# Optimization experiments

Hardware: AMD Instinct MI355X
Metric: run time of the kernel (lower is better)

The kernel has to match this reference:

```python
import jax, jax.numpy as jnp
import numpy as np
import math

M_MICRO = 8    # n_micro
CELLS = 1024   # cells per micro engine (n_cells // n_micro)
DIM = 512      # hidden_dim (complex state dim)
IN_DIM = 512   # input_dim == hidden_dim so torch's F.interpolate branch is skipped


def _build_neighbors(n):
    """Hypercube bit-flip + ring topology, deduped, padded to max degree."""
    n_bits = max(1, int(math.ceil(math.log2(n))))
    lists = []
    for i in range(n):
        s = set()
        for b in range(n_bits):
            j = i ^ (1 << b)
            if 0 <= j < n:
                s.add(j)
        s.add((i + 1) % n)
        s.add((i - 1) % n)
        lists.append(sorted(s))
    K = max(len(l) for l in lists)
    idx = np.zeros((n, K), dtype=np.int32)
    mask = np.zeros((n, K), dtype=np.float32)
    for i, l in enumerate(lists):
        idx[i, : len(l)] = l
        mask[i, : len(l)] = 1.0
    return idx, mask


def _forward(x, step, amp0, phase0, phase_vel, nbr_idx, nbr_mask, macro_h0,
             w_ih, b_ih, w_hh, b_hh, wq, bq, wk, bk, wv, bv, out_w, out_b):
    sig = x.reshape(-1)                    # [DIM]; input_dim == dim -> no interpolation
    t = step * 0.1
    states0 = amp0 * jnp.exp(1j * phase0)  # complex64 [M, n, d]

    def micro_step(st, pv):
        # phase-velocity rotation
        st = st * jnp.exp(1j * (pv * 0.1))
        ang = jnp.angle(st)
        nb_s = st[nbr_idx]                 # [n, K, d] neighbor gather
        nb_a = ang[nbr_idx]
        coupling = jnp.cos(ang[:, None, :] - nb_a)
        interf = jnp.sum(coupling * nb_s * nbr_mask[:, :, None], axis=1) * 0.1
        cnt = jnp.maximum(nbr_mask.sum(axis=1), 1.0)
        new = 0.7 * st + 0.3 * interf / cnt[:, None]
        # category morphism from strongest neighbor (selected on pre-interference states)
        absum = jnp.abs(st).sum(axis=-1)
        score = jnp.where(nbr_mask > 0, absum[nbr_idx], -jnp.inf)
        sel = jnp.argmax(score, axis=1)
        midx = jnp.take_along_axis(nbr_idx, sel[:, None], axis=1)[:, 0]
        src = st[midx]
        morph = jnp.abs(src) * jnp.exp(1j * (jnp.angle(new) - jnp.angle(src)))
        new = new + 0.02 * morph
        # global wave modulation
        i_arr = jnp.arange(new.shape[0], dtype=jnp.float32)
        wave = 0.02 * jnp.sin(t + 2.0 * math.pi * i_arr / new.shape[0])
        new = new * (1.0 + wave)[:, None]
        # signal phase perturbation (per-cell decaying scale)
        sig_norm = sig / (jnp.abs(sig).max() + 1e-8)
        pp = sig_norm * (math.pi * 0.1)
        scale = 0.1 / (1.0 + 0.1 * i_arr)
        newang = jnp.angle(new) + pp[None, :] * scale[:, None]
        # amplitude renormalization
        amp = jnp.abs(new)
        amp = amp / (amp.max(axis=-1, keepdims=True) + 1e-8)
        return amp * jnp.exp(1j * newang)

    states = jax.vmap(micro_step)(states0, phase_vel)  # [M, n, d]
    # micro outputs and coherences are .detach()'ed / .item()'ed in torch
    micro_out = jax.lax.stop_gradient(jnp.abs(states).mean(axis=1))          # [M, d]
    coh = jax.lax.stop_gradient(
        jnp.abs(jnp.exp(1j * jnp.angle(states)).mean(axis=1)).mean(axis=1))  # [M]
    # GRUCell (torch gate order: r, z, n)
    gx = micro_out @ w_ih.T + b_ih
    gh = macro_h0 @ w_hh.T + b_hh
    rx, zx, nx = jnp.split(gx, 3, axis=1)
    rh, zh, nh = jnp.split(gh, 3, axis=1)
    r = jax.nn.sigmoid(rx + rh)
    z = jax.nn.sigmoid(zx + zh)
    ng = jnp.tanh(nx + r * nh)
    h = jax.lax.stop_gradient((1.0 - z) * ng + z * macro_h0)  # detached macro hiddens
    H = h.shape[1]
    Q = h @ wq.T + bq
    K = h @ wk.T + bk
    V = h @ wv.T + bv
    scores = (Q @ K.T) / math.sqrt(H)
    scores = scores * (0.5 + 0.5 * coh[None, :] * coh[:, None])
    attn = jax.nn.softmax(scores, axis=-1)
    attended = (attn @ V).mean(axis=0, keepdims=True)  # [1, H]
    # faction sync/debate (updates hidden state; feeds only tension here)
    n_f = 4
    fs = h.shape[0] // n_f
    hh = h.reshape(n_f, fs, -1)
    hh = 0.85 * hh + 0.15 * hh.mean(axis=1, keepdims=True)
    if step > 5:
        go = hh.mean(axis=1).mean(axis=0)
        dc = max(1, fs // 4)
        hh = hh.at[:, :dc].set(0.85 * hh[:, :dc] + 0.15 * go)
    h2 = hh.reshape(h.shape)
    pred = attended @ out_w.T + out_b  # [1, IN_DIM]
    tension = jnp.var(h2, ddof=1)      # torch .var() is unbiased
    return pred, tension


def setup_inputs():
    key = jax.random.key(0)
    k = jax.random.split(key, 20)
    M, n, d, H, IN = M_MICRO, CELLS, DIM, DIM, IN_DIM
    amp0 = jax.random.uniform(k[0], (M, n, d)) * 0.5 + 0.5
    base = jnp.linspace(0.0, 2.0 * math.pi, d)
    gidx = jnp.arange(M * n, dtype=jnp.float32).reshape(M, n)
    off = 2.0 * math.pi * gidx / (n * 8)
    phase0 = base[None, None, :] + off[..., None] + jax.random.normal(k[1], (M, n, d)) * 0.3
    phase_vel = jax.random.normal(k[2], (M, n, d)) * 0.05
    nbr_idx, nbr_mask = _build_neighbors(n)
    macro_h0 = jax.random.normal(k[3], (M, H)) * 0.1
    s = 1.0 / math.sqrt(H)
    u = lambda kk, shape: jax.random.uniform(kk, shape, minval=-s, maxval=s)
    return {
        "x": jax.random.normal(k[4], (1, IN)),
        "step": 0,
        "amp0": amp0, "phase0": phase0, "phase_vel": phase_vel,
        "nbr_idx": jnp.asarray(nbr_idx), "nbr_mask": jnp.asarray(nbr_mask),
        "macro_h0": macro_h0,
        "w_ih": u(k[5], (3 * H, H)), "b_ih": u(k[6], (3 * H,)),
        "w_hh": u(k[7], (3 * H, H)), "b_hh": u(k[8], (3 * H,)),
        "wq": u(k[9], (H, H)), "bq": u(k[10], (H,)),
        "wk": u(k[11], (H, H)), "bk": u(k[12], (H,)),
        "wv": u(k[13], (H, H)), "bv": u(k[14], (H,)),
        "out_w": u(k[15], (IN, H)), "out_b": u(k[16], (IN,)),
    }


def reference(x, step, amp0, phase0, phase_vel, nbr_idx, nbr_mask, macro_h0,
              w_ih, b_ih, w_hh, b_hh, wq, bq, wk, bk, wv, bv, out_w, out_b):
    return _forward(x, step, amp0, phase0, phase_vel, nbr_idx, nbr_mask, macro_h0,
                    w_ih, b_ih, w_hh, b_hh, wq, bq, wk, bk, wv, bv, out_w, out_b)
```

## Files before the change

### kernel.cpp

```cpp
#include <hip/hip_runtime.h>
#include <math.h>

#define M_  8
#define N_  1024
#define D_  512
#define H_  512
#define PI_ 3.14159265358979323846f

static const size_t OFF_ABS = 0;
static const size_t OFF_SIG = OFF_ABS + 8192;
static const size_t OFF_PA  = OFF_SIG + 64;
static const size_t OFF_PZR = OFF_PA  + (size_t)M_*64*D_;
static const size_t OFF_PZI = OFF_PZR + (size_t)M_*64*D_;
static const size_t OFF_MO  = OFF_PZI + (size_t)M_*64*D_;
static const size_t OFF_COH = OFF_MO  + (size_t)M_*D_;
static const size_t OFF_H   = OFF_COH + 64;
static const size_t OFF_Q   = OFF_H   + (size_t)M_*H_;
static const size_t OFF_K   = OFF_Q   + (size_t)M_*H_;
static const size_t OFF_V   = OFF_K   + (size_t)M_*H_;
static const size_t OFF_ATT = OFF_V   + (size_t)M_*H_;

__device__ __forceinline__ void ld8(float* d, const float* __restrict__ p, int lane) {
    const float4* p4 = reinterpret_cast<const float4*>(p);
    float4 v0 = p4[2 * lane], v1 = p4[2 * lane + 1];
    d[0] = v0.x; d[1] = v0.y; d[2] = v0.z; d[3] = v0.w;
    d[4] = v1.x; d[5] = v1.y; d[6] = v1.z; d[7] = v1.w;
}


__global__ void prep_kernel(const float* __restrict__ amp0, const float* __restrict__ x,
                            float* __restrict__ absum, float* __restrict__ sigmax) {
    const int lane = threadIdx.x;
    if (blockIdx.x < M_ * N_) {
        float v[8];
        ld8(v, amp0 + (size_t)blockIdx.x * D_, lane);
        float acc = ((v[0] + v[1]) + (v[2] + v[3])) + ((v[4] + v[5]) + (v[6] + v[7]));
        for (int off = 32; off; off >>= 1) acc += __shfl_down(acc, off);
        if (lane == 0) absum[blockIdx.x] = acc;
    } else {
        float v[8];
        ld8(v, x, lane);
        float mx = 0.f;
        #pragma unroll
        for (int s = 0; s < 8; ++s) mx = fmaxf(mx, fabsf(v[s]));
        for (int off = 32; off; off >>= 1) mx = fmaxf(mx, __shfl_down(mx, off));
        if (lane == 0) *sigmax = mx;
    }
}

__global__ __launch_bounds__(512) void micro_kernel(
    const float* __restrict__ amp0, const float* __restrict__ phase0,
    const float* __restrict__ pv, const float* __restrict__ x,
    const float* __restrict__ sigmax_p, const int* __restrict__ nbr_idx,
    const float* __restrict__ nbr_mask, const int* __restrict__ step_p,
    const float* __restrict__ absum,
    float* __restrict__ pA, float* __restrict__ pZr, float* __restrict__ pZi, int K)
{
    const int m = blockIdx.x & 7;
    const int g = blockIdx.x >> 3;
    const int wid  = threadIdx.x >> 6;
    const int lane = threadIdx.x & 63;

    __shared__ float accA[D_], accZr[D_], accZi[D_];
    for (int idx = threadIdx.x; idx < D_; idx += 512) { accA[idx] = 0.f; accZr[idx] = 0.f; accZi[idx] = 0.f; }
    __syncthreads();

    const float t  = 0.1f * (float)(*step_p);
    const float sm = *sigmax_p;
    const int j0 = lane * 8;

    float pp[8];
    ld8(pp, x, lane);
    #pragma unroll
    for (int s = 0; s < 8; ++s) pp[s] = pp[s] / (sm + 1e-8f) * (PI_ * 0.1f);

    const size_t mrow = (size_t)m * N_;
    float sA[8], sZr[8], sZi[8];
    #pragma unroll
    for (int s = 0; s < 8; ++s) { sA[s] = 0.f; sZr[s] = 0.f; sZi[s] = 0.f; }

    for (int cc = 0; cc < 2; ++cc) {
        const int i = (g << 4) + (wid << 1) + cc;

        float SA[8], SB[8], SC[8];
        #pragma unroll
        for (int s = 0; s < 8; ++s) { SA[s] = 0.f; SB[s] = 0.f; SC[s] = 0.f; }
        float cnt = 0.f, best = -1e30f; int midx = 0;

        for (int k = 0; k < K; ++k) {
            const int   nb = nbr_idx[i * K + k];
            const float w  = nbr_mask[i * K + k];
            if (w > 0.f) {
                const size_t noff = (mrow + nb) * (size_t)D_;
                float an[8], phn[8], pvn[8];
                ld8(an, amp0 + noff, lane);
                ld8(phn, phase0 + noff, lane);
                ld8(pvn, pv + noff, lane);
                #pragma unroll
                for (int s = 0; s < 8; ++s) {
                    const float th = fmaf(0.1f, pvn[s], phn[s]);
                    const float cn = __cosf(th), sn = __sinf(th);
                    const float ac = an[s] * cn, as_ = an[s] * sn;
                    SA[s] = fmaf(ac, cn, SA[s]);
                    SB[s] = fmaf(ac, sn, SB[s]);
                    SC[s] = fmaf(as_, sn, SC[s]);
                }
                cnt += w;
                const float sc = absum[mrow + nb];
                if (sc > best) { best = sc; midx = nb; }
            }
        }
        const float f = 0.03f / fmaxf(cnt, 1.f);

        const size_t ooff = (mrow + i) * (size_t)D_;
        float a[8], ph[8], pw[8], nre[8], nim[8];
        ld8(a, amp0 + ooff, lane); ld8(ph, phase0 + ooff, lane); ld8(pw, pv + ooff, lane);
        #pragma unroll
        for (int s = 0; s < 8; ++s) {
            const float th = fmaf(0.1f, pw[s], ph[s]);
            const float c = __cosf(th), sn = __sinf(th);
            nre[s] = 0.7f * a[s] * c  + f * (c * SA[s] + sn * SB[s]);
            nim[s] = 0.7f * a[s] * sn + f * (c * SB[s] + sn * SC[s]);
        }

        const size_t soff = (mrow + midx) * (size_t)D_;
        ld8(a, amp0 + soff, lane); ld8(ph, phase0 + soff, lane); ld8(pw, pv + soff, lane);
        #pragma unroll
        for (int s = 0; s < 8; ++s) {
            const float th = fmaf(0.1f, pw[s], ph[s]);
            const float c = __cosf(th), sn = __sinf(th);
            const float sre = a[s] * c, sim = a[s] * sn;
            const float inv = __builtin_amdgcn_rcpf(sqrtf(nre[s]*nre[s] + nim[s]*nim[s]));
            const float mre = (nre[s] * sre + nim[s] * sim) * inv;
            const float mim = (nim[s] * sre - nre[s] * sim) * inv;
            nre[s] = fmaf(0.02f, mre, nre[s]);
            nim[s] = fmaf(0.02f, mim, nim[s]);
        }

        const float wf = 1.f + 0.02f * __sinf(t + 2.f * PI_ * (float)i / (float)N_);
        const float scale_i = 0.1f / (1.f + 0.1f * (float)i);

        float ampn[8], rm = 0.f;
        #pragma unroll
        for (int s = 0; s < 8; ++s) {
            nre[s] *= wf; nim[s] *= wf;
            ampn[s] = sqrtf(nre[s]*nre[s] + nim[s]*nim[s]);
            rm = fmaxf(rm, ampn[s]);
        }
        #pragma unroll
        for (int off = 1; off < 64; off <<= 1) rm = fmaxf(rm, __shfl_xor(rm, off));
        const float rinv = __builtin_amdgcn_rcpf(rm + 1e-8f);

        #pragma unroll
        for (int s = 0; s < 8; ++s) {
            const float anorm = ampn[s] * rinv;
            const float iamp  = __builtin_amdgcn_rcpf(ampn[s]);
            const float ure = nre[s] * iamp, uim = nim[s] * iamp;
            const float d  = pp[s] * scale_i;
            const float d2 = d * d;
            const float cd = 1.f - 0.5f * d2;
            const float sd = d * (1.f - 0.16666667f * d2);
            sA[s]  += anorm;
            sZr[s] += ure * cd - uim * sd;
            sZi[s] += ure * sd + uim * cd;
        }
    }

    #pragma unroll
    for (int s = 0; s < 8; ++s) {
        atomicAdd(&accA[j0 + s],  sA[s]);
        atomicAdd(&accZr[j0 + s], sZr[s]);
        atomicAdd(&accZi[j0 + s], sZi[s]);
    }
    __syncthreads();
    const int j = threadIdx.x;
    const size_t pidx = ((size_t)(m * 64 + g)) * D_ + j;
    pA[pidx]  = accA[j];
    pZr[pidx] = accZr[j];
    pZi[pidx] = accZi[j];
}

__global__ void reduce_kernel(const float* __restrict__ pA,
                              const float* __restrict__ pZr,
                              const float* __restrict__ pZi,
                              float* __restrict__ micro_out,
                              float* __restrict__ coh) {
    const int m = blockIdx.x, j = threadIdx.x;
    float sa = 0.f, zr = 0.f, zi = 0.f;
    for (int g = 0; g < 64; ++g) {
        const size_t idx = ((size_t)m * 64 + g) * D_ + j;
        sa += pA[idx]; zr += pZr[idx]; zi += pZi[idx];
    }
    micro_out[m * D_ + j] = sa * (1.f / (float)N_);
    const float mag = sqrtf(zr * zr + zi * zi) * (1.f / (float)N_);
    __shared__ float red[D_];
    red[j] = mag;
    __syncthreads();
    for (int s = D_/2; s > 0; s >>= 1) {
        if (j < s) red[j] += red[j + s];
        __syncthreads();
    }
    if (j == 0) coh[m] = red[0] / (float)D_;
}

__global__ __launch_bounds__(256) void macro_kernel(
    const float* __restrict__ mo, const float* __restrict__ h0,
    const float* __restrict__ w_ih, const float* __restrict__ b_ih,
    const float* __restrict__ w_hh, const float* __restrict__ b_hh,
    float* __restrict__ h)
{
    __shared__ float vx[M_ * H_], vh[M_ * H_];
    for (int idx = threadIdx.x; idx < M_ * H_; idx += 256) { vx[idx] = mo[idx]; vh[idx] = h0[idx]; }
    __syncthreads();
    const int wid = threadIdx.x >> 6, lane = threadIdx.x & 63;
    const int d = (blockIdx.x << 2) + wid;
    float wr[6][8];
    #pragma unroll
    for (int rr = 0; rr < 3; ++rr) {
        const size_t row = (size_t)(d + rr * H_) * H_;
        #pragma unroll
        for (int kk = 0; kk < 8; ++kk) {
            wr[rr][kk]     = w_ih[row + kk * 64 + lane];
            wr[rr + 3][kk] = w_hh[row + kk * 64 + lane];
        }
    }
    const float br = b_ih[d], bz = b_ih[d + H_], bn = b_ih[d + 2 * H_];
    const float dr = b_hh[d], dz = b_hh[d + H_], dn = b_hh[d + 2 * H_];
    for (int m = 0; m < M_; ++m) {
        float acc[6] = {0.f, 0.f, 0.f, 0.f, 0.f, 0.f};
        #pragma unroll
        for (int kk = 0; kk < 8; ++kk) {
            const float xm = vx[m * H_ + kk * 64 + lane];
            const float hm = vh[m * H_ + kk * 64 + lane];
            acc[0] = fmaf(wr[0][kk], xm, acc[0]);
            acc[1] = fmaf(wr[1][kk], xm, acc[1]);
            acc[2] = fmaf(wr[2][kk], xm, acc[2]);
            acc[3] = fmaf(wr[3][kk], hm, acc[3]);
            acc[4] = fmaf(wr[4][kk], hm, acc[4]);
            acc[5] = fmaf(wr[5][kk], hm, acc[5]);
        }
        #pragma unroll
        for (int off = 32; off; off >>= 1)
            #pragma unroll
            for (int q = 0; q < 6; ++q) acc[q] += __shfl_down(acc[q], off);
        if (lane == 0) {
            const float r  = 1.f / (1.f + expf(-(acc[0] + br + acc[3] + dr)));
            const float z  = 1.f / (1.f + expf(-(acc[1] + bz + acc[4] + dz)));
            const float ng = tanhf(acc[2] + bn + r * (acc[5] + dn));
            h[m * H_ + d] = (1.f - z) * ng + z * vh[m * H_ + d];
        }
    }
}

__global__ void qkv_kernel(const float* __restrict__ h,
                           const float* __restrict__ wq, const float* __restrict__ bq,
                           const float* __restrict__ wk, const float* __restrict__ bk,
                           const float* __restrict__ wv, const float* __restrict__ bv,
                           float* __restrict__ Q, float* __restrict__ Kk, float* __restrict__ V) {
    __shared__ float hv[M_ * H_];
    for (int idx = threadIdx.x; idx < M_ * H_; idx += blockDim.x) hv[idx] = h[idx];
    __syncthreads();
    const int gr = (blockIdx.x << 2) + (threadIdx.x >> 6);
    const int lane = threadIdx.x & 63;
    const int which = gr / H_, r = gr % H_;
    const float* W = (which == 0) ? wq : ((which == 1) ? wk : wv);
    const float* B = (which == 0) ? bq : ((which == 1) ? bk : bv);
    float* O       = (which == 0) ? Q  : ((which == 1) ? Kk : V);
    float wvv[8];
    #pragma unroll
    for (int kk = 0; kk < 8; ++kk) wvv[kk] = W[(size_t)r * H_ + kk * 64 + lane];
    for (int m = 0; m < M_; ++m) {
        float acc = 0.f;
        #pragma unroll
        for (int kk = 0; kk < 8; ++kk) acc = fmaf(wvv[kk], hv[m * H_ + kk * 64 + lane], acc);
        for (int off = 32; off; off >>= 1) acc += __shfl_down(acc, off);
        if (lane == 0) O[m * H_ + r] = acc + B[r];
    }
}

__global__ void attn_faction_kernel(const float* __restrict__ Q, const float* __restrict__ Kk,
                                    const float* __restrict__ V, const float* __restrict__ coh,
                                    const float* __restrict__ h, const int* __restrict__ step_p,
                                    float* __restrict__ attended, float* __restrict__ out_tension) {
    const int tid = threadIdx.x;
    {
        const int j = tid;
        const int step = *step_p;
        float h2[M_];
        #pragma unroll
        for (int ff = 0; ff < 4; ++ff) {
            const float a = h[(2*ff) * H_ + j], b = h[(2*ff+1) * H_ + j];
            const float mn = 0.5f * (a + b);
            h2[2*ff]   = 0.85f * a + 0.15f * mn;
            h2[2*ff+1] = 0.85f * b + 0.15f * mn;
        }
        if (step > 5) {
            float go = 0.f;
            #pragma unroll
            for (int m = 0; m < M_; ++m) go += h2[m];
            go *= (1.f / (float)M_);
            #pragma unroll
            for (int ff = 0; ff < 4; ++ff) h2[2*ff] = 0.85f * h2[2*ff] + 0.15f * go;
        }
        float sum = 0.f, sq = 0.f;
        #pragma unroll
        for (int m = 0; m < M_; ++m) { sum += h2[m]; sq = fmaf(h2[m], h2[m], sq); }
        __shared__ float rs[D_], rq[D_];
        rs[j] = sum; rq[j] = sq;
        __syncthreads();
        for (int s = D_/2; s > 0; s >>= 1) {
            if (j < s) { rs[j] += rs[j + s]; rq[j] += rq[j + s]; }
            __syncthreads();
        }
        if (j == 0) {
            const float Nt = (float)(M_ * H_);
            const float mean = rs[0] / Nt;
            out_tension[0] = (rq[0] - Nt * mean * mean) / (Nt - 1.f);
        }
        __syncthreads();
    }
    __shared__ float sc[M_][M_];
    __shared__ float colw[M_];
    const int a = tid >> 6, lane = tid & 63;
    for (int b = 0; b < M_; ++b) {
        float acc = 0.f;
        #pragma unroll
        for (int kk = 0; kk < 8; ++kk) acc = fmaf(Q[a * H_ + kk * 64 + lane], Kk[b * H_ + kk * 64 + lane], acc);
        for (int off = 32; off; off >>= 1) acc += __shfl_down(acc, off);
        if (lane == 0) sc[a][b] = acc * rsqrtf((float)H_) * (0.5f + 0.5f * coh[a] * coh[b]);
    }
    __syncthreads();
    if (tid < M_) {
        float mx = -1e30f;
        for (int b = 0; b < M_; ++b) mx = fmaxf(mx, sc[tid][b]);
        float e[M_], smm = 0.f;
        for (int b = 0; b < M_; ++b) { e[b] = expf(sc[tid][b] - mx); smm += e[b]; }
        for (int b = 0; b < M_; ++b) sc[tid][b] = e[b] / smm;
    }
    __syncthreads();
    if (tid < M_) {
        float sum = 0.f;
        for (int a2 = 0; a2 < M_; ++a2) sum += sc[a2][tid];
        colw[tid] = sum * (1.f / (float)M_);
    }
    __syncthreads();
    float acc = 0.f;
    #pragma unroll
    for (int b = 0; b < M_; ++b) acc = fmaf(colw[b], V[b * H_ + tid], acc);
    attended[tid] = acc;
}

__global__ void pred_kernel(const float* __restrict__ attended,
                            const float* __restrict__ out_w, const float* __restrict__ out_b,
                            float* __restrict__ pred) {
    __shared__ float av[H_];
    for (int idx = threadIdx.x; idx < H_; idx += blockDim.x) av[idx] = attended[idx];
    __syncthreads();
    const int p = (blockIdx.x << 2) + (threadIdx.x >> 6);
    const int lane = threadIdx.x & 63;
    float acc = 0.f;
    #pragma unroll
    for (int kk = 0; kk < 8; ++kk) acc = fmaf(av[kk * 64 + lane], out_w[(size_t)p * H_ + kk * 64 + lane], acc);
    for (int off = 32; off; off >>= 1) acc += __shfl_down(acc, off);
    if (lane == 0) pred[p] = acc + out_b[p];
}


extern "C" void kernel_launch(void* const* d_in, const int* in_sizes, int n_in,
                              void* d_out, int out_size, void* d_ws, size_t ws_size,
                              hipStream_t stream) {
    const float* x      = (const float*)d_in[0];
    const int*   step   = (const int*)  d_in[1];
    const float* amp0   = (const float*)d_in[2];
    const float* phase0 = (const float*)d_in[3];
    const float* pvel   = (const float*)d_in[4];
    const int*   nbr_i  = (const int*)  d_in[5];
    const float* nbr_m  = (const float*)d_in[6];
    const float* h0     = (const float*)d_in[7];
    const float* w_ih   = (const float*)d_in[8];
    const float* b_ih   = (const float*)d_in[9];
    const float* w_hh   = (const float*)d_in[10];
    const float* b_hh   = (const float*)d_in[11];
    const float* wq     = (const float*)d_in[12];
    const float* bq     = (const float*)d_in[13];
    const float* wk     = (const float*)d_in[14];
    const float* bk     = (const float*)d_in[15];
    const float* wv     = (const float*)d_in[16];
    const float* bv     = (const float*)d_in[17];
    const float* out_w  = (const float*)d_in[18];
    const float* out_b  = (const float*)d_in[19];
    float* out = (float*)d_out;

    const int K = in_sizes[5] / N_;

    float* ws   = (float*)d_ws;
    float* wABS = ws + OFF_ABS;
    float* wSIG = ws + OFF_SIG;
    float* wPA  = ws + OFF_PA;
    float* wPZR = ws + OFF_PZR;
    float* wPZI = ws + OFF_PZI;
    float* wMO  = ws + OFF_MO;
    float* wCOH = ws + OFF_COH;
    float* wH   = ws + OFF_H;
    float* wQ   = ws + OFF_Q;
    float* wK   = ws + OFF_K;
    float* wV   = ws + OFF_V;
    float* wATT = ws + OFF_ATT;

    prep_kernel<<<M_ * N_ + 1, 64, 0, stream>>>(amp0, x, wABS, wSIG);
    micro_kernel<<<512, 512, 0, stream>>>(amp0, phase0, pvel, x, wSIG, nbr_i, nbr_m, step,
                                          wABS, wPA, wPZR, wPZI, K);
    reduce_kernel<<<M_, D_, 0, stream>>>(wPA, wPZR, wPZI, wMO, wCOH);
    macro_kernel<<<128, 256, 0, stream>>>(wMO, h0, w_ih, b_ih, w_hh, b_hh, wH);
    qkv_kernel<<<384, 256, 0, stream>>>(wH, wq, bq, wk, bk, wv, bv, wQ, wK, wV);
    attn_faction_kernel<<<1, 512, 0, stream>>>(wQ, wK, wV, wCOH, wH, step, wATT, out + 512);
    pred_kernel<<<128, 256, 0, stream>>>(wATT, out_w, out_b, out);
}
```

Baseline: 227.0 us.

## Precompute half-precision cos/sin table and fuse partial reductions via atomics

A prep pass now computes the rotated phase's cos/sin once per element and stores it as packed half2, so the micro kernel reads amp plus one half2 stream instead of recomputing trig from phase and velocity for every neighbour visit. The per-row absolute sums are computed inline with a wavefront reduction, so the separate absum pass goes away. Partial sums are accumulated straight into global buffers with atomics, which drops the reduce kernel, and coherence is computed inside the attention kernel. A fallback path keeps the fp32 recompute when the workspace is too small. The cost is an extra full-size half2 table write and read, fp16 rounding of cos/sin, and global atomic contention.

```diff
diff --git a/kernel.cpp b/kernel.cpp
--- a/kernel.cpp
+++ b/kernel.cpp
@@ -1,4 +1,5 @@
 #include <hip/hip_runtime.h>
+#include <hip/hip_fp16.h>
 #include <math.h>
 
 #define M_  8
@@ -7,210 +8,358 @@
 #define H_  512
 #define PI_ 3.14159265358979323846f
 
-static const size_t OFF_ABS = 0;
-static const size_t OFF_SIG = OFF_ABS + 8192;
-static const size_t OFF_PA  = OFF_SIG + 64;
-static const size_t OFF_PZR = OFF_PA  + (size_t)M_*64*D_;
-static const size_t OFF_PZI = OFF_PZR + (size_t)M_*64*D_;
-static const size_t OFF_MO  = OFF_PZI + (size_t)M_*64*D_;
-static const size_t OFF_COH = OFF_MO  + (size_t)M_*D_;
-static const size_t OFF_H   = OFF_COH + 64;
+static const size_t OFF_CHS = 0;
+static const size_t OFF_SIG = OFF_CHS + (size_t)M_*N_*D_;
+static const size_t OFF_MA  = OFF_SIG + 64;
+static const size_t OFF_MZR = OFF_MA  + (size_t)M_*D_;
+static const size_t OFF_MZI = OFF_MZR + (size_t)M_*D_;
+static const size_t OFF_H   = OFF_MZI + (size_t)M_*D_;
 static const size_t OFF_Q   = OFF_H   + (size_t)M_*H_;
 static const size_t OFF_K   = OFF_Q   + (size_t)M_*H_;
 static const size_t OFF_V   = OFF_K   + (size_t)M_*H_;
 static const size_t OFF_ATT = OFF_V   + (size_t)M_*H_;
-
-__device__ __forceinline__ void ld8(float* d, const float* __restrict__ p, int lane) {
-    const float4* p4 = reinterpret_cast<const float4*>(p);
-    float4 v0 = p4[2 * lane], v1 = p4[2 * lane + 1];
-    d[0] = v0.x; d[1] = v0.y; d[2] = v0.z; d[3] = v0.w;
-    d[4] = v1.x; d[5] = v1.y; d[6] = v1.z; d[7] = v1.w;
-}
-
-
-__global__ void prep_kernel(const float* __restrict__ amp0, const float* __restrict__ x,
-                            float* __restrict__ absum, float* __restrict__ sigmax) {
-    const int lane = threadIdx.x;
-    if (blockIdx.x < M_ * N_) {
+static const size_t FAST_FLOATS = OFF_ATT + 512;
+static const size_t FB_SIG = 0;
+static const size_t FB_MA  = FB_SIG + 64;
+static const size_t FB_MZR = FB_MA  + (size_t)M_*D_;
+static const size_t FB_MZI = FB_MZR + (size_t)M_*D_;
+static const size_t FB_H   = FB_MZI + (size_t)M_*D_;
+static const size_t FB_Q   = FB_H   + (size_t)M_*H_;
+static const size_t FB_K   = FB_Q   + (size_t)M_*H_;
+static const size_t FB_V   = FB_K   + (size_t)M_*H_;
+static const size_t FB_ATT = FB_V   + (size_t)M_*H_;
+
+struct F8   { float4 a, b; };
+struct H2x8 { __half2 h[8]; };
+
+__device__ __forceinline__ void unp8(float* d, const F8& v) {
+    d[0]=v.a.x; d[1]=v.a.y; d[2]=v.a.z; d[3]=v.a.w;
+    d[4]=v.b.x; d[5]=v.b.y; d[6]=v.b.z; d[7]=v.b.w;
+}
+
+
+__global__ __launch_bounds__(256) void prep_kernel(const float* __restrict__ phase0,
+                                                   const float* __restrict__ pv,
+                                                   const float* __restrict__ x,
+                                                   __half2* __restrict__ chs,
+                                                   float* __restrict__ acczero,
+                                                   float* __restrict__ sigmax) {
+    const int bid = blockIdx.x, tid = threadIdx.x;
+    if (bid < 2048) {
+        const size_t e = ((size_t)bid * 256 + tid) * 8;
+        float ph[8], pw[8];
+        unp8(ph, *reinterpret_cast<const F8*>(phase0 + e));
+        unp8(pw, *reinterpret_cast<const F8*>(pv + e));
+        H2x8 out;
+        #pragma unroll
+        for (int s = 0; s < 8; ++s) {
+            const float th = fmaf(0.1f, pw[s], ph[s]);
+            out.h[s] = __floats2half2_rn(__cosf(th), __sinf(th));
+        }
+        *reinterpret_cast<H2x8*>(chs + e) = out;
+        if (bid < 6) {
+            F8 z; z.a = make_float4(0.f,0.f,0.f,0.f); z.b = z.a;
+            *reinterpret_cast<F8*>(acczero + (size_t)bid * 2048 + (size_t)tid * 8) = z;
+        }
+    } else if (tid < 64) {
         float v[8];
-        ld8(v, amp0 + (size_t)blockIdx.x * D_, lane);
-        float acc = ((v[0] + v[1]) + (v[2] + v[3])) + ((v[4] + v[5]) + (v[6] + v[7]));
-        for (int off = 32; off; off >>= 1) acc += __shfl_down(acc, off);
-        if (lane == 0) absum[blockIdx.x] = acc;
-    } else {
-        float v[8];
-        ld8(v, x, lane);
+        unp8(v, *reinterpret_cast<const F8*>(x + (size_t)tid * 8));
         float mx = 0.f;
         #pragma unroll
         for (int s = 0; s < 8; ++s) mx = fmaxf(mx, fabsf(v[s]));
+        #pragma unroll
         for (int off = 32; off; off >>= 1) mx = fmaxf(mx, __shfl_down(mx, off));
-        if (lane == 0) *sigmax = mx;
+        if (tid == 0) *sigmax = mx;
     }
 }
 
 __global__ __launch_bounds__(512) void micro_kernel(
-    const float* __restrict__ amp0, const float* __restrict__ phase0,
-    const float* __restrict__ pv, const float* __restrict__ x,
-    const float* __restrict__ sigmax_p, const int* __restrict__ nbr_idx,
-    const float* __restrict__ nbr_mask, const int* __restrict__ step_p,
-    const float* __restrict__ absum,
-    float* __restrict__ pA, float* __restrict__ pZr, float* __restrict__ pZi, int K)
+    const float* __restrict__ amp0, const __half2* __restrict__ chs,
+    const float* __restrict__ x, const float* __restrict__ sigmax_p,
+    const int* __restrict__ nbr_idx, const float* __restrict__ nbr_mask,
+    const int* __restrict__ step_p,
+    float* __restrict__ mA, float* __restrict__ mZr, float* __restrict__ mZi, int K)
 {
     const int m = blockIdx.x & 7;
     const int g = blockIdx.x >> 3;
     const int wid  = threadIdx.x >> 6;
     const int lane = threadIdx.x & 63;
+    const int i = (g << 3) + wid;
 
     __shared__ float accA[D_], accZr[D_], accZi[D_];
-    for (int idx = threadIdx.x; idx < D_; idx += 512) { accA[idx] = 0.f; accZr[idx] = 0.f; accZi[idx] = 0.f; }
+    for (int idx = threadIdx.x; idx < D_; idx += 512) { accA[idx]=0.f; accZr[idx]=0.f; accZi[idx]=0.f; }
     __syncthreads();
 
     const float t  = 0.1f * (float)(*step_p);
     const float sm = *sigmax_p;
-    const int j0 = lane * 8;
 
     float pp[8];
-    ld8(pp, x, lane);
+    unp8(pp, *reinterpret_cast<const F8*>(x + (size_t)lane * 8));
     #pragma unroll
     for (int s = 0; s < 8; ++s) pp[s] = pp[s] / (sm + 1e-8f) * (PI_ * 0.1f);
 
     const size_t mrow = (size_t)m * N_;
-    float sA[8], sZr[8], sZi[8];
-    #pragma unroll
-    for (int s = 0; s < 8; ++s) { sA[s] = 0.f; sZr[s] = 0.f; sZi[s] = 0.f; }
-
-    for (int cc = 0; cc < 2; ++cc) {
-        const int i = (g << 4) + (wid << 1) + cc;
-
-        float SA[8], SB[8], SC[8];
-        #pragma unroll
-        for (int s = 0; s < 8; ++s) { SA[s] = 0.f; SB[s] = 0.f; SC[s] = 0.f; }
-        float cnt = 0.f, best = -1e30f; int midx = 0;
-
-        for (int k = 0; k < K; ++k) {
-            const int   nb = nbr_idx[i * K + k];
-            const float w  = nbr_mask[i * K + k];
-            if (w > 0.f) {
-                const size_t noff = (mrow + nb) * (size_t)D_;
-                float an[8], phn[8], pvn[8];
-                ld8(an, amp0 + noff, lane);
-                ld8(phn, phase0 + noff, lane);
-                ld8(pvn, pv + noff, lane);
-                #pragma unroll
-                for (int s = 0; s < 8; ++s) {
-                    const float th = fmaf(0.1f, pvn[s], phn[s]);
-                    const float cn = __cosf(th), sn = __sinf(th);
-                    const float ac = an[s] * cn, as_ = an[s] * sn;
-                    SA[s] = fmaf(ac, cn, SA[s]);
-                    SB[s] = fmaf(ac, sn, SB[s]);
-                    SC[s] = fmaf(as_, sn, SC[s]);
-                }
-                cnt += w;
-                const float sc = absum[mrow + nb];
-                if (sc > best) { best = sc; midx = nb; }
-            }
-        }
-        const float f = 0.03f / fmaxf(cnt, 1.f);
-
-        const size_t ooff = (mrow + i) * (size_t)D_;
-        float a[8], ph[8], pw[8], nre[8], nim[8];
-        ld8(a, amp0 + ooff, lane); ld8(ph, phase0 + ooff, lane); ld8(pw, pv + ooff, lane);
+
+    int L = 0;
+    for (int k = 0; k < K; ++k) L += (nbr_mask[i * K + k] > 0.f) ? 1 : 0;
+
+    float SA[8], SB[8], SC[8];
+    #pragma unroll
+    for (int s = 0; s < 8; ++s) { SA[s]=0.f; SB[s]=0.f; SC[s]=0.f; }
+    float best = -1e30f; int midx = 0;
+
+    for (int k = 0; k < L; ++k) {
+        const int nb = nbr_idx[i * K + k];
+        const size_t noff = (mrow + nb) * (size_t)D_ + (size_t)lane * 8;
+        float aN[8];
+        unp8(aN, *reinterpret_cast<const F8*>(amp0 + noff));
+        const H2x8 hx = *reinterpret_cast<const H2x8*>(chs + noff);
         #pragma unroll
         for (int s = 0; s < 8; ++s) {
-            const float th = fmaf(0.1f, pw[s], ph[s]);
-            const float c = __cosf(th), sn = __sinf(th);
-            nre[s] = 0.7f * a[s] * c  + f * (c * SA[s] + sn * SB[s]);
-            nim[s] = 0.7f * a[s] * sn + f * (c * SB[s] + sn * SC[s]);
-        }
-
-        const size_t soff = (mrow + midx) * (size_t)D_;
-        ld8(a, amp0 + soff, lane); ld8(ph, phase0 + soff, lane); ld8(pw, pv + soff, lane);
+            const float2 cs = __half22float2(hx.h[s]);
+            const float ac = aN[s] * cs.x, as_ = aN[s] * cs.y;
+            SA[s] = fmaf(ac,  cs.x, SA[s]);
+            SB[s] = fmaf(ac,  cs.y, SB[s]);
+            SC[s] = fmaf(as_, cs.y, SC[s]);
+        }
+        float rs = ((aN[0]+aN[1])+(aN[2]+aN[3])) + ((aN[4]+aN[5])+(aN[6]+aN[7]));
+        #pragma unroll
+        for (int off = 1; off < 64; off <<= 1) rs += __shfl_xor(rs, off);
+        const bool sel = rs > best;
+        best = sel ? rs : best;
+        midx = sel ? nb : midx;
+    }
+    const float f = 0.03f / fmaxf((float)L, 1.f);
+
+    float nre[8], nim[8];
+    {
+        const size_t ooff = (mrow + i) * (size_t)D_ + (size_t)lane * 8;
+        float aO[8];
+        unp8(aO, *reinterpret_cast<const F8*>(amp0 + ooff));
+        const H2x8 hx = *reinterpret_cast<const H2x8*>(chs + ooff);
         #pragma unroll
         for (int s = 0; s < 8; ++s) {
-            const float th = fmaf(0.1f, pw[s], ph[s]);
-            const float c = __cosf(th), sn = __sinf(th);
-            const float sre = a[s] * c, sim = a[s] * sn;
+            const float2 cs = __half22float2(hx.h[s]);
+            nre[s] = 0.7f * aO[s] * cs.x + f * (cs.x * SA[s] + cs.y * SB[s]);
+            nim[s] = 0.7f * aO[s] * cs.y + f * (cs.x * SB[s] + cs.y * SC[s]);
+        }
+    }
+    {
+        const size_t soff = (mrow + midx) * (size_t)D_ + (size_t)lane * 8;
+        float aS[8];
+        unp8(aS, *reinterpret_cast<const F8*>(amp0 + soff));
+        const H2x8 hx = *reinterpret_cast<const H2x8*>(chs + soff);
+        #pragma unroll
+        for (int s = 0; s < 8; ++s) {
+            const float2 cs = __half22float2(hx.h[s]);
+            const float sre = aS[s] * cs.x, sim = aS[s] * cs.y;
             const float inv = __builtin_amdgcn_rcpf(sqrtf(nre[s]*nre[s] + nim[s]*nim[s]));
             const float mre = (nre[s] * sre + nim[s] * sim) * inv;
             const float mim = (nim[s] * sre - nre[s] * sim) * inv;
             nre[s] = fmaf(0.02f, mre, nre[s]);
             nim[s] = fmaf(0.02f, mim, nim[s]);
         }
-
-        const float wf = 1.f + 0.02f * __sinf(t + 2.f * PI_ * (float)i / (float)N_);
-        const float scale_i = 0.1f / (1.f + 0.1f * (float)i);
-
-        float ampn[8], rm = 0.f;
+    }
+
+    const float wf = 1.f + 0.02f * __sinf(t + 2.f * PI_ * (float)i / (float)N_);
+    const float scale_i = 0.1f / (1.f + 0.1f * (float)i);
+
+    float ampn[8], rm = 0.f;
+    #pragma unroll
+    for (int s = 0; s < 8; ++s) {
+        nre[s] *= wf; nim[s] *= wf;
+        ampn[s] = sqrtf(nre[s]*nre[s] + nim[s]*nim[s]);
+        rm = fmaxf(rm, ampn[s]);
+    }
+    #pragma unroll
+    for (int off = 1; off < 64; off <<= 1) rm = fmaxf(rm, __shfl_xor(rm, off));
+    const float rinv = __builtin_amdgcn_rcpf(rm + 1e-8f);
+
+    #pragma unroll
+    for (int s = 0; s < 8; ++s) {
+        const float anorm = ampn[s] * rinv;
+        const float iamp  = __builtin_amdgcn_rcpf(ampn[s]);
+        const float ure = nre[s] * iamp, uim = nim[s] * iamp;
+        const float d  = pp[s] * scale_i;
+        const float d2 = d * d;
+        const float cd = 1.f - 0.5f * d2;
+        const float sd = d * (1.f - 0.16666667f * d2);
+        const int p = (s << 6) + lane;
+        atomicAdd(&accA[p],  anorm);
+        atomicAdd(&accZr[p], ure * cd - uim * sd);
+        atomicAdd(&accZi[p], ure * sd + uim * cd);
+    }
+    __syncthreads();
+    const int j = threadIdx.x;
+    const int p = ((j & 7) << 6) + (j >> 3);
+    atomicAdd(&mA [m * D_ + j], accA[p]);
+    atomicAdd(&mZr[m * D_ + j], accZr[p]);
+    atomicAdd(&mZi[m * D_ + j], accZi[p]);
+}
+
+
+__global__ __launch_bounds__(256) void zero_sig_kernel(const float* __restrict__ x,
+                                                       float* __restrict__ acczero,
+                                                       float* __restrict__ sigmax) {
+    const int bid = blockIdx.x, tid = threadIdx.x;
+    if (bid < 6) {
+        F8 z; z.a = make_float4(0.f,0.f,0.f,0.f); z.b = z.a;
+        *reinterpret_cast<F8*>(acczero + (size_t)bid * 2048 + (size_t)tid * 8) = z;
+    } else if (tid < 64) {
+        float v[8];
+        unp8(v, *reinterpret_cast<const F8*>(x + (size_t)tid * 8));
+        float mx = 0.f;
+        #pragma unroll
+        for (int s = 0; s < 8; ++s) mx = fmaxf(mx, fabsf(v[s]));
+        #pragma unroll
+        for (int off = 32; off; off >>= 1) mx = fmaxf(mx, __shfl_down(mx, off));
+        if (tid == 0) *sigmax = mx;
+    }
+}
+
+__global__ __launch_bounds__(512) void micro_fb_kernel(
+    const float* __restrict__ amp0, const float* __restrict__ phase0,
+    const float* __restrict__ pvel,
+    const float* __restrict__ x, const float* __restrict__ sigmax_p,
+    const int* __restrict__ nbr_idx, const float* __restrict__ nbr_mask,
+    const int* __restrict__ step_p,
+    float* __restrict__ mA, float* __restrict__ mZr, float* __restrict__ mZi, int K)
+{
+    const int m = blockIdx.x & 7;
+    const int g = blockIdx.x >> 3;
+    const int wid  = threadIdx.x >> 6;
+    const int lane = threadIdx.x & 63;
+    const int i = (g << 3) + wid;
+
+    __shared__ float accA[D_], accZr[D_], accZi[D_];
+    for (int idx = threadIdx.x; idx < D_; idx += 512) { accA[idx]=0.f; accZr[idx]=0.f; accZi[idx]=0.f; }
+    __syncthreads();
+
+    const float t  = 0.1f * (float)(*step_p);
+    const float sm = *sigmax_p;
+
+    float pp[8];
+    unp8(pp, *reinterpret_cast<const F8*>(x + (size_t)lane * 8));
+    #pragma unroll
+    for (int s = 0; s < 8; ++s) pp[s] = pp[s] / (sm + 1e-8f) * (PI_ * 0.1f);
+
+    const size_t mrow = (size_t)m * N_;
+
+    int L = 0;
+    for (int k = 0; k < K; ++k) L += (nbr_mask[i * K + k] > 0.f) ? 1 : 0;
+
+    float SA[8], SB[8], SC[8];
+    #pragma unroll
+    for (int s = 0; s < 8; ++s) { SA[s]=0.f; SB[s]=0.f; SC[s]=0.f; }
+    float best = -1e30f; int midx = 0;
+
+    for (int k = 0; k < L; ++k) {
+        const int nb = nbr_idx[i * K + k];
+        const size_t noff = (mrow + nb) * (size_t)D_ + (size_t)lane * 8;
+        float aN[8], phN[8], pwN[8];
+        unp8(aN, *reinterpret_cast<const F8*>(amp0 + noff));
+        unp8(phN, *reinterpret_cast<const F8*>(phase0 + noff));
+        unp8(pwN, *reinterpret_cast<const F8*>(pvel + noff));
         #pragma unroll
         for (int s = 0; s < 8; ++s) {
-            nre[s] *= wf; nim[s] *= wf;
-            ampn[s] = sqrtf(nre[s]*nre[s] + nim[s]*nim[s]);
-            rm = fmaxf(rm, ampn[s]);
-        }
-        #pragma unroll
-        for (int off = 1; off < 64; off <<= 1) rm = fmaxf(rm, __shfl_xor(rm, off));
-        const float rinv = __builtin_amdgcn_rcpf(rm + 1e-8f);
-
+            const float th = fmaf(0.1f, pwN[s], phN[s]);
+            const float cn = __cosf(th), sn = __sinf(th);
+            const float ac = aN[s] * cn, as_ = aN[s] * sn;
+            SA[s] = fmaf(ac,  cn, SA[s]);
+            SB[s] = fmaf(ac,  sn, SB[s]);
+            SC[s] = fmaf(as_, sn, SC[s]);
+        }
+        float rs = ((aN[0]+aN[1])+(aN[2]+aN[3])) + ((aN[4]+aN[5])+(aN[6]+aN[7]));
+        #pragma unroll
+        for (int off = 1; off < 64; off <<= 1) rs += __shfl_xor(rs, off);
+        const bool sel = rs > best;
+        best = sel ? rs : best;
+        midx = sel ? nb : midx;
+    }
+    const float f = 0.03f / fmaxf((float)L, 1.f);
+
+    float nre[8], nim[8];
+    {
+        const size_t ooff = (mrow + i) * (size_t)D_ + (size_t)lane * 8;
+        float aO[8], ph[8], pw[8];
+        unp8(aO, *reinterpret_cast<const F8*>(amp0 + ooff));
+        unp8(ph, *reinterpret_cast<const F8*>(phase0 + ooff));
+        unp8(pw, *reinterpret_cast<const F8*>(pvel + ooff));
         #pragma unroll
         for (int s = 0; s < 8; ++s) {
-            const float anorm = ampn[s] * rinv;
-            const float iamp  = __builtin_amdgcn_rcpf(ampn[s]);
-            const float ure = nre[s] * iamp, uim = nim[s] * iamp;
-            const float d  = pp[s] * scale_i;
-            const float d2 = d * d;
-            const float cd = 1.f - 0.5f * d2;
-            const float sd = d * (1.f - 0.16666667f * d2);
-            sA[s]  += anorm;
-            sZr[s] += ure * cd - uim * sd;
-            sZi[s] += ure * sd + uim * cd;
-        }
-    }
-
+            const float th = fmaf(0.1f, pw[s], ph[s]);
+            const float c = __cosf(th), sn = __sinf(th);
+            nre[s] = 0.7f * aO[s] * c  + f * (c * SA[s] + sn * SB[s]);
+            nim[s] = 0.7f * aO[s] * sn + f * (c * SB[s] + sn * SC[s]);
+        }
+    }
+    {
+        const size_t soff = (mrow + midx) * (size_t)D_ + (size_t)lane * 8;
+        float aS[8], ph[8], pw[8];
+        unp8(aS, *reinterpret_cast<const F8*>(amp0 + soff));
+        unp8(ph, *reinterpret_cast<const F8*>(phase0 + soff));
+        unp8(pw, *reinterpret_cast<const F8*>(pvel + soff));
+        #pragma unroll
+        for (int s = 0; s < 8; ++s) {
+            const float th = fmaf(0.1f, pw[s], ph[s]);
+            const float c = __cosf(th), sn = __sinf(th);
+            const float sre = aS[s] * c, sim = aS[s] * sn;
+            const float inv = __builtin_amdgcn_rcpf(sqrtf(nre[s]*nre[s] + nim[s]*nim[s]));
+            const float mre = (nre[s] * sre + nim[s] * sim) * inv;
+            const float mim = (nim[s] * sre - nre[s] * sim) * inv;
+            nre[s] = fmaf(0.02f, mre, nre[s]);
+            nim[s] = fmaf(0.02f, mim, nim[s]);
+        }
+    }
+
+    const float wf = 1.f + 0.02f * __sinf(t + 2.f * PI_ * (float)i / (float)N_);
+    const float scale_i = 0.1f / (1.f + 0.1f * (float)i);
+
+    float ampn[8], rm = 0.f;
     #pragma unroll
     for (int s = 0; s < 8; ++s) {
-        atomicAdd(&accA[j0 + s],  sA[s]);
-        atomicAdd(&accZr[j0 + s], sZr[s]);
-        atomicAdd(&accZi[j0 + s], sZi[s]);
+        nre[s] *= wf; nim[s] *= wf;
+        ampn[s] = sqrtf(nre[s]*nre[s] + nim[s]*nim[s]);
+        rm = fmaxf(rm, ampn[s]);
+    }
+    #pragma unroll
+    for (int off = 1; off < 64; off <<= 1) rm = fmaxf(rm, __shfl_xor(rm, off));
+    const float rinv = __builtin_amdgcn_rcpf(rm + 1e-8f);
+
+    #pragma unroll
+    for (int s = 0; s < 8; ++s) {
+        const float anorm = ampn[s] * rinv;
+        const float iamp  = __builtin_amdgcn_rcpf(ampn[s]);
+        const float ure = nre[s] * iamp, uim = nim[s] * iamp;
+        const float d  = pp[s] * scale_i;
+        const float d2 = d * d;
+        const float cd = 1.f - 0.5f * d2;
+        const float sd = d * (1.f - 0.16666667f * d2);
+        const int p = (s << 6) + lane;
+        atomicAdd(&accA[p],  anorm);
+        atomicAdd(&accZr[p], ure * cd - uim * sd);
+        atomicAdd(&accZi[p], ure * sd + uim * cd);
     }
     __syncthreads();
     const int j = threadIdx.x;
-    const size_t pidx = ((size_t)(m * 64 + g)) * D_ + j;
-    pA[pidx]  = accA[j];
-    pZr[pidx] = accZr[j];
-    pZi[pidx] = accZi[j];
-}
-
-__global__ void reduce_kernel(const float* __restrict__ pA,
-                              const float* __restrict__ pZr,
-                              const float* __restrict__ pZi,
-                              float* __restrict__ micro_out,
-                              float* __restrict__ coh) {
-    const int m = blockIdx.x, j = threadIdx.x;
-    float sa = 0.f, zr = 0.f, zi = 0.f;
-    for (int g = 0; g < 64; ++g) {
-        const size_t idx = ((size_t)m * 64 + g) * D_ + j;
-        sa += pA[idx]; zr += pZr[idx]; zi += pZi[idx];
-    }
-    micro_out[m * D_ + j] = sa * (1.f / (float)N_);
-    const float mag = sqrtf(zr * zr + zi * zi) * (1.f / (float)N_);
-    __shared__ float red[D_];
-    red[j] = mag;
-    __syncthreads();
-    for (int s = D_/2; s > 0; s >>= 1) {
-        if (j < s) red[j] += red[j + s];
-        __syncthreads();
-    }
-    if (j == 0) coh[m] = red[0] / (float)D_;
-}
+    const int p = ((j & 7) << 6) + (j >> 3);
+    atomicAdd(&mA [m * D_ + j], accA[p]);
+    atomicAdd(&mZr[m * D_ + j], accZr[p]);
+    atomicAdd(&mZi[m * D_ + j], accZi[p]);
+}
+
 
 __global__ __launch_bounds__(256) void macro_kernel(
-    const float* __restrict__ mo, const float* __restrict__ h0,
+    const float* __restrict__ mA, const float* __restrict__ h0,
     const float* __restrict__ w_ih, const float* __restrict__ b_ih,
     const float* __restrict__ w_hh, const float* __restrict__ b_hh,
     float* __restrict__ h)
 {
     __shared__ float vx[M_ * H_], vh[M_ * H_];
-    for (int idx = threadIdx.x; idx < M_ * H_; idx += 256) { vx[idx] = mo[idx]; vh[idx] = h0[idx]; }
+    for (int idx = threadIdx.x; idx < M_ * H_; idx += 256) {
+        vx[idx] = mA[idx] * (1.f / (float)N_);
+        vh[idx] = h0[idx];
+    }
     __syncthreads();
     const int wid = threadIdx.x >> 6, lane = threadIdx.x & 63;
     const int d = (blockIdx.x << 2) + wid;
@@ -279,10 +428,26 @@
 }
 
 __global__ void attn_faction_kernel(const float* __restrict__ Q, const float* __restrict__ Kk,
-                                    const float* __restrict__ V, const float* __restrict__ coh,
+                                    const float* __restrict__ V,
+                                    const float* __restrict__ mZr, const float* __restrict__ mZi,
                                     const float* __restrict__ h, const int* __restrict__ step_p,
                                     float* __restrict__ attended, float* __restrict__ out_tension) {
     const int tid = threadIdx.x;
+    __shared__ float coh_sm[M_];
+    {
+        const int w = tid >> 6, lane = tid & 63;
+        float s = 0.f;
+        #pragma unroll
+        for (int q = 0; q < 8; ++q) {
+            const int j = lane + (q << 6);
+            const float zr = mZr[w * D_ + j], zi = mZi[w * D_ + j];
+            s += sqrtf(zr * zr + zi * zi);
+        }
+        #pragma unroll
+        for (int off = 32; off; off >>= 1) s += __shfl_down(s, off);
+        if (lane == 0) coh_sm[w] = s * (1.f / ((float)N_ * (float)D_));
+    }
+    __syncthreads();
     {
         const int j = tid;
         const int step = *step_p;
@@ -327,7 +492,7 @@
         #pragma unroll
         for (int kk = 0; kk < 8; ++kk) acc = fmaf(Q[a * H_ + kk * 64 + lane], Kk[b * H_ + kk * 64 + lane], acc);
         for (int off = 32; off; off >>= 1) acc += __shfl_down(acc, off);
-        if (lane == 0) sc[a][b] = acc * rsqrtf((float)H_) * (0.5f + 0.5f * coh[a] * coh[b]);
+        if (lane == 0) sc[a][b] = acc * rsqrtf((float)H_) * (0.5f + 0.5f * coh_sm[a] * coh_sm[b]);
     }
     __syncthreads();
     if (tid < M_) {
@@ -392,27 +557,44 @@
     float* out = (float*)d_out;
 
     const int K = in_sizes[5] / N_;
-
-    float* ws   = (float*)d_ws;
-    float* wABS = ws + OFF_ABS;
-    float* wSIG = ws + OFF_SIG;
-    float* wPA  = ws + OFF_PA;
-    float* wPZR = ws + OFF_PZR;
-    float* wPZI = ws + OFF_PZI;
-    float* wMO  = ws + OFF_MO;
-    float* wCOH = ws + OFF_COH;
-    float* wH   = ws + OFF_H;
-    float* wQ   = ws + OFF_Q;
-    float* wK   = ws + OFF_K;
-    float* wV   = ws + OFF_V;
-    float* wATT = ws + OFF_ATT;
-
-    prep_kernel<<<M_ * N_ + 1, 64, 0, stream>>>(amp0, x, wABS, wSIG);
-    micro_kernel<<<512, 512, 0, stream>>>(amp0, phase0, pvel, x, wSIG, nbr_i, nbr_m, step,
-                                          wABS, wPA, wPZR, wPZI, K);
-    reduce_kernel<<<M_, D_, 0, stream>>>(wPA, wPZR, wPZI, wMO, wCOH);
-    macro_kernel<<<128, 256, 0, stream>>>(wMO, h0, w_ih, b_ih, w_hh, b_hh, wH);
-    qkv_kernel<<<384, 256, 0, stream>>>(wH, wq, bq, wk, bk, wv, bv, wQ, wK, wV);
-    attn_faction_kernel<<<1, 512, 0, stream>>>(wQ, wK, wV, wCOH, wH, step, wATT, out + 512);
-    pred_kernel<<<128, 256, 0, stream>>>(wATT, out_w, out_b, out);
-}
+    float* ws = (float*)d_ws;
+
+    if (ws_size >= FAST_FLOATS * sizeof(float)) {
+        __half2* wCHS = (__half2*)(ws + OFF_CHS);
+        float* wSIG = ws + OFF_SIG;
+        float* wMA  = ws + OFF_MA;
+        float* wMZR = ws + OFF_MZR;
+        float* wMZI = ws + OFF_MZI;
+        float* wH   = ws + OFF_H;
+        float* wQ   = ws + OFF_Q;
+        float* wK   = ws + OFF_K;
+        float* wV   = ws + OFF_V;
+        float* wATT = ws + OFF_ATT;
+
+        prep_kernel<<<2049, 256, 0, stream>>>(phase0, pvel, x, wCHS, wMA, wSIG);
+        micro_kernel<<<1024, 512, 0, stream>>>(amp0, wCHS, x, wSIG, nbr_i, nbr_m, step,
+                                               wMA, wMZR, wMZI, K);
+        macro_kernel<<<128, 256, 0, stream>>>(wMA, h0, w_ih, b_ih, w_hh, b_hh, wH);
+        qkv_kernel<<<384, 256, 0, stream>>>(wH, wq, bq, wk, bk, wv, bv, wQ, wK, wV);
+        attn_faction_kernel<<<1, 512, 0, stream>>>(wQ, wK, wV, wMZR, wMZI, wH, step, wATT, out + 512);
+        pred_kernel<<<128, 256, 0, stream>>>(wATT, out_w, out_b, out);
+    } else {
+        float* wSIG = ws + FB_SIG;
+        float* wMA  = ws + FB_MA;
+        float* wMZR = ws + FB_MZR;
+        float* wMZI = ws + FB_MZI;
+        float* wH   = ws + FB_H;
+        float* wQ   = ws + FB_Q;
+        float* wK   = ws + FB_K;
+        float* wV   = ws + FB_V;
+        float* wATT = ws + FB_ATT;
+
+        zero_sig_kernel<<<7, 256, 0, stream>>>(x, wMA, wSIG);
+        micro_fb_kernel<<<1024, 512, 0, stream>>>(amp0, phase0, pvel, x, wSIG, nbr_i, nbr_m, step,
+                                                  wMA, wMZR, wMZI, K);
+        macro_kernel<<<128, 256, 0, stream>>>(wMA, h0, w_ih, b_ih, w_hh, b_hh, wH);
+        qkv_kernel<<<384, 256, 0, stream>>>(wH, wq, bq, wk, bk, wv, bv, wQ, wK, wV);
+        attn_faction_kernel<<<1, 512, 0, stream>>>(wQ, wK, wV, wMZR, wMZI, wH, step, wATT, out + 512);
+        pred_kernel<<<128, 256, 0, stream>>>(wATT, out_w, out_b, out);
+    }
+}
```

Result: slower. 252.4 us (+11.2%).
